# Kernel optimization log

Measured on AMD Instinct MI355X. Metric: run time of the kernel, lower is better.

## Reference

```python
import jax, jax.numpy as jnp
import numpy as np
from jax import lax

B, S, D, H = 8, 1024, 512, 8
K = 25  # moving-average kernel
EPS = 1e-6


def setup_inputs() -> dict:
    key = jax.random.key(0)
    ks = jax.random.split(key, 8)

    def dense_w(k, din, dout):
        return (jax.random.normal(k, (din, dout), jnp.float32) / np.sqrt(din).astype(np.float32))

    return {
        "x": jax.random.normal(ks[0], (B, S, D), jnp.float32),
        "wq": dense_w(ks[1], D, D), "bq": jnp.zeros((D,), jnp.float32),
        "wk": dense_w(ks[2], D, D), "bk": jnp.zeros((D,), jnp.float32),
        "wv": dense_w(ks[3], D, D), "bv": jnp.zeros((D,), jnp.float32),
        "wo": dense_w(ks[4], D, D), "bo": jnp.zeros((D,), jnp.float32),
        "w1": dense_w(ks[5], D, 4 * D), "b1": jnp.zeros((4 * D,), jnp.float32),
        "w2": dense_w(ks[6], 4 * D, D), "b2": jnp.zeros((D,), jnp.float32),
        "g1": jnp.ones((D,), jnp.float32), "be1": jnp.zeros((D,), jnp.float32),
        "g2": jnp.ones((D,), jnp.float32), "be2": jnp.zeros((D,), jnp.float32),
        "g3": jnp.ones((D,), jnp.float32), "be3": jnp.zeros((D,), jnp.float32),
        "num_heads": H,
    }


def _moving_avg(x):
    # TF AveragePooling1D(pool=K, stride=1, padding='same'): divisor excludes padding.
    s = lax.reduce_window(x, 0.0, lax.add, (1, K, 1), (1, 1, 1), 'SAME')
    cnt = lax.reduce_window(jnp.ones((1, x.shape[1], 1), x.dtype), 0.0, lax.add,
                            (1, K, 1), (1, 1, 1), 'SAME')
    return s / cnt


def _layernorm(x, g, b):
    m = jnp.mean(x, -1, keepdims=True)
    v = jnp.var(x, -1, keepdims=True)
    return (x - m) * jax.lax.rsqrt(v + EPS) * g + b


def _auto_correlation(x, wq, bq, wk, bk, wv, bv, wo, bo, num_heads):
    b, s, d = x.shape
    dp = d // num_heads
    def split_heads(t):
        return t.reshape(b, s, num_heads, dp).transpose(0, 2, 1, 3)  # [B,H,S,dp]
    q = split_heads(x @ wq + bq)
    k = split_heads(x @ wk + bk)
    v = split_heads(x @ wv + bv)
    # Faithful to source: rfft over innermost (depth) axis, fft_length = 2*S.
    qf = jnp.fft.rfft(q, n=2 * s, axis=-1)
    kf = jnp.fft.rfft(k, n=2 * s, axis=-1)
    corr = jnp.fft.irfft(qf * jnp.conj(kf), n=2 * s, axis=-1)[..., :s]  # [B,H,S,S]
    scale = 1.0 / np.sqrt(dp).astype(np.float32)
    attn = jax.nn.softmax(scale * corr, axis=-1)
    out = jnp.einsum('bhst,bhtd->bhsd', attn, v)
    out = out.transpose(0, 2, 1, 3).reshape(b, s, d)
    return out @ wo + bo


def reference(x, wq, bq, wk, bk, wv, bv, wo, bo, w1, b1, w2, b2,
              g1, be1, g2, be2, g3, be3, num_heads):
    trend_init = _moving_avg(x)
    seasonal_init = x - trend_init
    attn_out = _auto_correlation(seasonal_init, wq, bq, wk, bk, wv, bv, wo, bo, num_heads)
    out1 = _layernorm(attn_out + seasonal_init, g1, be1)
    ffn = jax.nn.relu(out1 @ w1 + b1) @ w2 + b2
    seasonal_out = _layernorm(out1 + ffn, g2, be2) + seasonal_init
    trend2 = _moving_avg(seasonal_out)
    seasonal_final = seasonal_out - trend2
    x_out = seasonal_final + (trend2 + trend_init)
    return _layernorm(x_out, g3, be3)
```

## Files before the change

### kernel.cpp

```cpp
#include <hip/hip_runtime.h>
#include <cstdint>


typedef float f32x4 __attribute__((ext_vector_type(4)));
typedef __bf16 bf16x8 __attribute__((ext_vector_type(8)));
typedef _Float16 h2t __attribute__((ext_vector_type(2)));
typedef unsigned short u16;
typedef unsigned int u32;
typedef u32 u32x4 __attribute__((ext_vector_type(4)));

__device__ __forceinline__ u16 f2bf(float f) {
  unsigned int u = __float_as_uint(f);
  u = (u + 0x7FFFu + ((u >> 16) & 1u)) >> 16;
  return (u16)u;
}

__device__ __forceinline__ float bf2f(u16 b) { return __uint_as_float((u32)b << 16); }

__device__ __forceinline__ u16 f2h(float f) {
  _Float16 hv = (_Float16)f;
  u16 b;
  __builtin_memcpy(&b, &hv, 2);
  return b;
}

__device__ __forceinline__ float dot2h(u32 qp, u32 kp_, float c) {
#if __has_builtin(__builtin_amdgcn_fdot2)
  return __builtin_amdgcn_fdot2(__builtin_bit_cast(h2t, qp),
                                __builtin_bit_cast(h2t, kp_), c, false);
#else
  h2t q = __builtin_bit_cast(h2t, qp), k = __builtin_bit_cast(h2t, kp_);
  c = fmaf((float)q.x, (float)k.x, c);
  return fmaf((float)q.y, (float)k.y, c);
#endif
}

__device__ __forceinline__ void gload_lds16(const void* g, void* l) {
  __builtin_amdgcn_global_load_lds((__attribute__((address_space(1))) void*)g,
                                   (__attribute__((address_space(3))) void*)l,
                                   16, 0, 0);
}

__global__ __launch_bounds__(256) void prep_kernel(
    const float* __restrict__ wq, const float* __restrict__ wk,
    const float* __restrict__ wv, const float* __restrict__ wo,
    const float* __restrict__ w1, const float* __restrict__ w2,
    const float* __restrict__ bq, const float* __restrict__ bk,
    u16* __restrict__ wqkt, u16* __restrict__ wvt, u16* __restrict__ wot,
    u16* __restrict__ w1t, u16* __restrict__ w2t, float* __restrict__ qkbias,
    const float* __restrict__ x, u16* __restrict__ seas_bf,
    u16* __restrict__ a64, float* __restrict__ srow) {
  __shared__ float tile[32][33];
  int i = blockIdx.x;
  int tid = threadIdx.x;
  int tx = tid & 31, ty = tid >> 5;
  if (i >= 3076) {
    int blk = i - 3076;
    int sc = blk & 127, b = blk >> 7;
    int d = tid * 2;
    const float* xb = x + (size_t)b * 1024 * 512 + d;
    int s0 = sc * 8;
    int lo = max(s0 - 12, 0), hi = min(s0 + 12, 1023);
    float sx = 0.f, sy = 0.f;
    for (int j = lo; j <= hi; ++j) {
      float2 v = *(const float2*)&xb[(size_t)j * 512];
      sx += v.x;
      sy += v.y;
    }
    float ax = 0.f, ay = 0.f;
#pragma unroll
    for (int s = s0; s < s0 + 8; ++s) {
      int l2 = max(s - 12, 0), h2 = min(s + 12, 1023);
      float invc = 1.f / (float)(h2 - l2 + 1);
      float2 xv = *(const float2*)&xb[(size_t)s * 512];
      float sex = xv.x - sx * invc;
      float sey = xv.y - sy * invc;
      size_t idx = (size_t)(b * 1024 + s) * 512 + d;
      u32 pk = (u32)f2bf(sex) | ((u32)f2bf(sey) << 16);
      *(u32*)&seas_bf[idx] = pk;
      if (s < 64) *(u32*)&a64[(size_t)(b * 64 + s) * 512 + d] = pk;
      ax += sex;
      ay += sey;
      if (s - 12 >= 0) {
        float2 v = *(const float2*)&xb[(size_t)(s - 12) * 512];
        sx -= v.x;
        sy -= v.y;
      }
      if (s + 13 <= 1023) {
        float2 v = *(const float2*)&xb[(size_t)(s + 13) * 512];
        sx += v.x;
        sy += v.y;
      }
    }
    atomicAdd(&srow[b * 512 + d], ax);
    atomicAdd(&srow[b * 512 + d + 1], ay);
    return;
  }
  if (i >= 3072) {
    int idx = (i - 3072) * 256 + tid;
    qkbias[idx] = idx < 512 ? bq[idx] : bk[idx - 512];
    return;
  }
  const float* src;
  u16* dst;
  int R, C, bx, by;
  if (i < 1024) {
    int w = i >> 8, l = i & 255;
    src = (w == 0 ? wq : w == 1 ? wk : w == 2 ? wv : wo);
    dst = (w == 0 ? wqkt : w == 1 ? wqkt + 512 * 512 : w == 2 ? wvt : wot);
    R = 512; C = 512; bx = l & 15; by = l >> 4;
  } else if (i < 2048) {
    int l = i - 1024;
    src = w1; dst = w1t; R = 512; C = 2048; bx = l & 15; by = l >> 4;
  } else {
    int l = i - 2048;
    src = w2; dst = w2t; R = 2048; C = 512; bx = l & 63; by = l >> 6;
  }
  int r0 = bx * 32, c0 = by * 32;
#pragma unroll
  for (int k = 0; k < 4; ++k)
    tile[ty + 8 * k][tx] = src[(size_t)(r0 + ty + 8 * k) * C + c0 + tx];
  __syncthreads();
#pragma unroll
  for (int k = 0; k < 4; ++k)
    dst[(size_t)(c0 + ty + 8 * k) * R + r0 + tx] = f2bf(tile[tx][ty + 8 * k]);
}

__global__ __launch_bounds__(256) void vsum_kernel(
    const float* __restrict__ srow, const float* __restrict__ wv,
    const float* __restrict__ bv, float* __restrict__ vsum) {
  int blk = blockIdx.x;
  int b = blk >> 1;
  int n = (blk & 1) * 256 + threadIdx.x;
  float a0 = 0.f, a1 = 0.f, a2 = 0.f, a3 = 0.f;
  float a4 = 0.f, a5 = 0.f, a6 = 0.f, a7 = 0.f;
  const float* sr = srow + b * 512;
  for (int k = 0; k < 512; k += 8) {
    a0 = fmaf(sr[k + 0], wv[(size_t)(k + 0) * 512 + n], a0);
    a1 = fmaf(sr[k + 1], wv[(size_t)(k + 1) * 512 + n], a1);
    a2 = fmaf(sr[k + 2], wv[(size_t)(k + 2) * 512 + n], a2);
    a3 = fmaf(sr[k + 3], wv[(size_t)(k + 3) * 512 + n], a3);
    a4 = fmaf(sr[k + 4], wv[(size_t)(k + 4) * 512 + n], a4);
    a5 = fmaf(sr[k + 5], wv[(size_t)(k + 5) * 512 + n], a5);
    a6 = fmaf(sr[k + 6], wv[(size_t)(k + 6) * 512 + n], a6);
    a7 = fmaf(sr[k + 7], wv[(size_t)(k + 7) * 512 + n], a7);
  }
  vsum[b * 512 + n] = ((a0 + a1) + (a2 + a3)) + ((a4 + a5) + (a6 + a7)) + 1024.f * bv[n];
}

template <int RELU, int OMODE, int KSPLIT>
__global__ __launch_bounds__(512, 1) void gemm8p_kernel(
    const u16* __restrict__ A, const u16* __restrict__ Bt,
    const float* __restrict__ bias, void* __restrict__ Cv, void* __restrict__ Cv2,
    int M, int N, int K) {
  __shared__ u16 As[3][2][256 * 32];
  __shared__ u16 Bs[3][2][128 * 32];
  const int tid = threadIdx.x;
  const int wid = tid >> 6, lane = tid & 63;
  const int wm = wid >> 2, wn = wid & 3;
  const int la = lane & 15, lg = lane >> 4;
  int nwg = gridDim.x * gridDim.y;
  int lin = blockIdx.y * gridDim.x + blockIdx.x;
  int swz = (lin & 7) * (nwg >> 3) + (lin >> 3);
  int bx = swz / gridDim.y, by = swz % gridDim.y;
  const int row0 = bx * 256, col0 = by * 128;
  const int z = (KSPLIT > 1) ? (int)blockIdx.z : 0;
  const int kbeg = z * (K / KSPLIT);
  const int nt = (K / KSPLIT) / 64;
  f32x4 acc[8][2] = {};

  auto stageh = [&](int buf, int h, int k0) {
    int kh = k0 + h * 32;
    {
      int p = tid, r = p >> 2, cg = (p & 3) ^ ((r >> 1) & 3);
      gload_lds16(A + (size_t)(row0 + r) * K + kh + cg * 8,
                  ((char*)&As[buf][h][0]) + p * 16);
    }
    {
      int p = tid + 512, r = p >> 2, cg = (p & 3) ^ ((r >> 1) & 3);
      gload_lds16(A + (size_t)(row0 + r) * K + kh + cg * 8,
                  ((char*)&As[buf][h][0]) + p * 16);
    }
    {
      int p = tid, r = p >> 2, cg = (p & 3) ^ ((r >> 1) & 3);
      gload_lds16(Bt + (size_t)(col0 + r) * K + kh + cg * 8,
                  ((char*)&Bs[buf][h][0]) + p * 16);
    }
  };

  stageh(0, 0, kbeg);
  stageh(0, 1, kbeg);
  stageh(1, 0, kbeg + 64);
  stageh(1, 1, kbeg + 64);
  asm volatile("s_waitcnt vmcnt(6)" ::: "memory");
  __builtin_amdgcn_s_barrier();
  __builtin_amdgcn_sched_barrier(0);

  for (int t = 0; t < nt; ++t) {
    const int buf = t % 3;
    const int nbuf = (t + 2) % 3;
    const bool pre = (t + 2 < nt);
#pragma unroll
    for (int h = 0; h < 2; ++h) {
      bf16x8 af[8], bf[2];
#pragma unroll
      for (int mf = 0; mf < 8; ++mf) {
        int r = wm * 128 + mf * 16 + la;
        int cp = lg ^ ((r >> 1) & 3);
        af[mf] = *(const bf16x8*)&As[buf][h][r * 32 + cp * 8];
      }
#pragma unroll
      for (int nf = 0; nf < 2; ++nf) {
        int r = wn * 32 + nf * 16 + la;
        int cp = lg ^ ((r >> 1) & 3);
        bf[nf] = *(const bf16x8*)&Bs[buf][h][r * 32 + cp * 8];
      }
      if (pre) stageh(nbuf, h, kbeg + (t + 2) * 64);
      __builtin_amdgcn_sched_barrier(0);
      __builtin_amdgcn_s_barrier();
      __builtin_amdgcn_s_setprio(1);
#pragma unroll
      for (int mf = 0; mf < 8; ++mf)
#pragma unroll
        for (int nf = 0; nf < 2; ++nf)
          acc[mf][nf] = __builtin_amdgcn_mfma_f32_16x16x32_bf16(af[mf], bf[nf], acc[mf][nf], 0, 0, 0);
      __builtin_amdgcn_s_setprio(0);
      __builtin_amdgcn_sched_barrier(0);
      if (h == 0) __builtin_amdgcn_s_barrier();
    }
    if (pre)
      asm volatile("s_waitcnt vmcnt(6)" ::: "memory");
    else if (t + 1 < nt)
      asm volatile("s_waitcnt vmcnt(0)" ::: "memory");
    __builtin_amdgcn_s_barrier();
    __builtin_amdgcn_sched_barrier(0);
  }

  void* Cout = (z == 0) ? Cv : Cv2;
#pragma unroll
  for (int mf = 0; mf < 8; ++mf) {
    int r = row0 + wm * 128 + mf * 16 + lg * 4;
#pragma unroll
    for (int nf = 0; nf < 2; ++nf) {
      int cc = col0 + wn * 32 + nf * 16 + la;
      float bvv = (z == 0) ? bias[cc] : 0.f;
#pragma unroll
      for (int j = 0; j < 4; ++j) {
        float v = acc[mf][nf][j] + bvv;
        if (RELU) v = fmaxf(v, 0.f);
        if constexpr (OMODE == 1)
          ((u16*)Cout)[(size_t)(r + j) * N + cc] = f2bf(v);
        else
          ((u16*)Cout)[(size_t)(r + j) * N + cc] = f2h(v);
      }
    }
  }
}

template <int RELU, int KSPLIT>
__global__ __launch_bounds__(512, 1) void gemmfp_kernel(
    const u16* __restrict__ A, const u16* __restrict__ Bt,
    const float* __restrict__ bias, u16* __restrict__ C0, u16* __restrict__ C1,
    u16* __restrict__ C2, u16* __restrict__ C3, int M, int N, int K) {
  __shared__ u16 As[2][2][256 * 32];
  __shared__ u16 Bs[2][2][256 * 32];
  const int tid = threadIdx.x;
  const int wid = tid >> 6, lane = tid & 63;
  const int wm = wid >> 2, wn = wid & 3;
  const int la = lane & 15, lg = lane >> 4;
  int nwg = gridDim.x * gridDim.y;
  int lin = blockIdx.y * gridDim.x + blockIdx.x;
  int swz = (lin & 7) * (nwg >> 3) + (lin >> 3);
  int bx = swz / gridDim.y, by = swz % gridDim.y;
  const int row0 = bx * 256, col0 = by * 256;
  const int z = (KSPLIT > 1) ? (int)blockIdx.z : 0;
  const int kbeg = z * (K / KSPLIT);
  const int nt = (K / KSPLIT) / 64;
  f32x4 acc[8][4] = {};

  auto stageA = [&](int d, int s, int k0) {
#pragma unroll
    for (int j = 0; j < 2; ++j) {
      int p = tid + j * 512;
      int r = p >> 2, cg = (p & 3) ^ ((r >> 1) & 3);
      gload_lds16(A + (size_t)(row0 + r) * K + k0 + s * 32 + cg * 8,
                  ((char*)&As[d][s][0]) + p * 16);
    }
  };
  auto stageB = [&](int d, int s, int k0) {
#pragma unroll
    for (int j = 0; j < 2; ++j) {
      int p = tid + j * 512;
      int r = p >> 2, cg = (p & 3) ^ ((r >> 1) & 3);
      gload_lds16(Bt + (size_t)(col0 + r) * K + k0 + s * 32 + cg * 8,
                  ((char*)&Bs[d][s][0]) + p * 16);
    }
  };

  stageA(0, 0, kbeg);
  stageB(0, 0, kbeg);
  stageA(0, 1, kbeg);
  stageB(0, 1, kbeg);
  asm volatile("s_waitcnt vmcnt(0)" ::: "memory");
  __builtin_amdgcn_s_barrier();
  __builtin_amdgcn_sched_barrier(0);

  for (int t = 0; t < nt; ++t) {
    const int d = t & 1, nd = d ^ 1;
    const int k1 = kbeg + (t + 1) * 64;
    const bool pre = (t + 1 < nt);
    bf16x8 af[8], bf[2];
#pragma unroll
    for (int s = 0; s < 2; ++s) {
#pragma unroll
      for (int mf = 0; mf < 8; ++mf) {
        int r = wm * 128 + mf * 16 + la;
        int cp = lg ^ ((r >> 1) & 3);
        af[mf] = *(const bf16x8*)(((const char*)&As[d][s][0]) + r * 64 + cp * 16);
      }
#pragma unroll
      for (int nf = 0; nf < 2; ++nf) {
        int r = wn * 64 + nf * 16 + la;
        int cp = lg ^ ((r >> 1) & 3);
        bf[nf] = *(const bf16x8*)(((const char*)&Bs[d][s][0]) + r * 64 + cp * 16);
      }
      if (pre) stageA(nd, s, k1);
      __builtin_amdgcn_sched_barrier(0);
      __builtin_amdgcn_s_barrier();
      asm volatile("s_waitcnt lgkmcnt(0)" ::: "memory");
      __builtin_amdgcn_sched_barrier(0);
      __builtin_amdgcn_s_setprio(1);
#pragma unroll
      for (int mf = 0; mf < 8; ++mf)
#pragma unroll
        for (int nf = 0; nf < 2; ++nf)
          acc[mf][nf] = __builtin_amdgcn_mfma_f32_16x16x32_bf16(af[mf], bf[nf], acc[mf][nf], 0, 0, 0);
      __builtin_amdgcn_s_setprio(0);
      __builtin_amdgcn_sched_barrier(0);
      __builtin_amdgcn_s_barrier();
#pragma unroll
      for (int nf = 0; nf < 2; ++nf) {
        int r = wn * 64 + (nf + 2) * 16 + la;
        int cp = lg ^ ((r >> 1) & 3);
        bf[nf] = *(const bf16x8*)(((const char*)&Bs[d][s][0]) + r * 64 + cp * 16);
      }
      if (pre) stageB(nd, s, k1);
      __builtin_amdgcn_sched_barrier(0);
      if (pre)
        asm volatile("s_waitcnt vmcnt(4)" ::: "memory");
      else
        asm volatile("s_waitcnt vmcnt(0)" ::: "memory");
      __builtin_amdgcn_s_barrier();
      asm volatile("s_waitcnt lgkmcnt(0)" ::: "memory");
      __builtin_amdgcn_sched_barrier(0);
      __builtin_amdgcn_s_setprio(1);
#pragma unroll
      for (int mf = 0; mf < 8; ++mf)
#pragma unroll
        for (int nf = 0; nf < 2; ++nf)
          acc[mf][nf + 2] = __builtin_amdgcn_mfma_f32_16x16x32_bf16(af[mf], bf[nf], acc[mf][nf + 2], 0, 0, 0);
      __builtin_amdgcn_s_setprio(0);
      __builtin_amdgcn_sched_barrier(0);
      __builtin_amdgcn_s_barrier();
    }
  }

  u16* Cout = (z == 0) ? C0 : (z == 1) ? C1 : (z == 2) ? C2 : C3;
#pragma unroll
  for (int mf = 0; mf < 8; ++mf) {
    int r = row0 + wm * 128 + mf * 16 + lg * 4;
#pragma unroll
    for (int nf = 0; nf < 4; ++nf) {
      int cc = col0 + wn * 64 + nf * 16 + la;
      float bvv = (z == 0) ? bias[cc] : 0.f;
#pragma unroll
      for (int j = 0; j < 4; ++j) {
        float v = acc[mf][nf][j] + bvv;
        if (RELU) v = fmaxf(v, 0.f);
        Cout[(size_t)(r + j) * N + cc] = f2bf(v);
      }
    }
  }
}

__global__ __launch_bounds__(256, 6) void gemm_v_kernel(
    const u16* __restrict__ A, const u16* __restrict__ Bt,
    const float* __restrict__ bias, u16* __restrict__ Cv, int M, int N, int K) {
  constexpr int BK = 32;
  __shared__ u16 As[2][128 * BK];
  __shared__ u16 Bs[2][64 * BK];
  const int tid = threadIdx.x;
  const int wid = tid >> 6, lane = tid & 63;
  const int wm = wid >> 1, wn = wid & 1;
  const int la = lane & 15, lg = lane >> 4;
  const int row0 = blockIdx.x * 128, col0 = blockIdx.y * 64;
  const int ksteps = K / BK;
  f32x4 acc[4][2] = {};

  auto stage = [&](int buf, int k0) {
    {
      int p = tid, r = p >> 2, cg = (p & 3) ^ ((r >> 1) & 3);
      gload_lds16(A + (size_t)(row0 + r) * K + k0 + cg * 8, ((char*)As[buf]) + p * 16);
    }
    {
      int p = tid + 256, r = p >> 2, cg = (p & 3) ^ ((r >> 1) & 3);
      gload_lds16(A + (size_t)(row0 + r) * K + k0 + cg * 8, ((char*)As[buf]) + p * 16);
    }
    {
      int p = tid, r = p >> 2, cg = (p & 3) ^ ((r >> 1) & 3);
      gload_lds16(Bt + (size_t)(col0 + r) * K + k0 + cg * 8, ((char*)Bs[buf]) + p * 16);
    }
  };

  stage(0, 0);
  __syncthreads();
  for (int t = 0; t < ksteps; ++t) {
    const int cur = t & 1;
    if (t + 1 < ksteps) stage(cur ^ 1, (t + 1) * BK);
    bf16x8 af[4], bfr[2];
#pragma unroll
    for (int m = 0; m < 4; ++m) {
      int r = wm * 64 + m * 16 + la;
      int cp = lg ^ ((r >> 1) & 3);
      af[m] = *(const bf16x8*)(((const char*)As[cur]) + r * 64 + cp * 16);
    }
#pragma unroll
    for (int n = 0; n < 2; ++n) {
      int r = wn * 32 + n * 16 + la;
      int cp = lg ^ ((r >> 1) & 3);
      bfr[n] = *(const bf16x8*)(((const char*)Bs[cur]) + r * 64 + cp * 16);
    }
#pragma unroll
    for (int m = 0; m < 4; ++m)
#pragma unroll
      for (int n = 0; n < 2; ++n)
        acc[m][n] = __builtin_amdgcn_mfma_f32_16x16x32_bf16(af[m], bfr[n], acc[m][n], 0, 0, 0);
    __syncthreads();
  }

#pragma unroll
  for (int m = 0; m < 4; ++m) {
    int r = row0 + wm * 64 + m * 16 + lg * 4;
#pragma unroll
    for (int n = 0; n < 2; ++n) {
      int cc = col0 + wn * 32 + n * 16 + la;
      float bvv = bias[cc];
#pragma unroll
      for (int j = 0; j < 4; ++j) {
        float v = acc[m][n][j] + bvv;
        int rr = r + j;
        int bb = rr >> 6, tt = rr & 63, hh = cc >> 6, dd = cc & 63;
        Cv[(((size_t)bb * 8 + hh) * 64 + dd) * 64 + tt] = f2bf(v);
      }
    }
  }
}

__global__ __launch_bounds__(256) void attn_mfma_kernel(
    const u16* __restrict__ qk, const u16* __restrict__ v64t,
    const float* __restrict__ vsum, u16* __restrict__ attn_bf) {
  __shared__ u32 qE[16][64];
  __shared__ u32 qO[16][64];
  __shared__ u32 kp[16][32];
  __shared__ u16 coef[16][64];
  __shared__ u16 vtt[64][64];
  __shared__ float zc[16];
  __shared__ float Vs[64];
  int bid = blockIdx.x;
  int scnk = bid & 63, h = (bid >> 6) & 7, b = bid >> 9;
  int tid = threadIdx.x, wid = tid >> 6, lane = tid & 63;
  int bh = b * 8 + h;
  int row0 = b * 1024 + scnk * 16;

  {
    int p = tid, r = p >> 3, cc = p & 7;
    gload_lds16(v64t + ((size_t)bh * 4096 + r * 64 + ((cc ^ (r & 7)) * 8)),
                ((char*)vtt) + p * 16);
    p = tid + 256; r = p >> 3; cc = p & 7;
    gload_lds16(v64t + ((size_t)bh * 4096 + r * 64 + ((cc ^ (r & 7)) * 8)),
                ((char*)vtt) + p * 16);
  }
  for (int idx = tid; idx < 512; idx += 256) {
    int s = idx >> 5, j = (idx & 31) + 32;
    qE[s][j] = 0;
  }
  {
    if (tid < 128) {
      int s = tid >> 3, c = tid & 7;
      size_t grow = ((size_t)(row0 + s)) * 1024 + h * 64;
      *(f32x4*)&qE[s][c * 4] = *(const f32x4*)&qk[grow + c * 8];
    } else {
      int t2 = tid - 128;
      int s = t2 >> 3, c = t2 & 7;
      size_t grow = ((size_t)(row0 + s)) * 1024 + 512 + h * 64;
      *(f32x4*)&kp[s][c * 4] = *(const f32x4*)&qk[grow + c * 8];
    }
  }
  if (tid < 64) Vs[tid] = vsum[b * 512 + h * 64 + tid];
  __syncthreads();
  for (int idx = tid; idx < 512; idx += 256) {
    int s = idx >> 5, j = idx & 31;
    u32 a = qE[s][j], b2 = qE[s][j + 1];
    qO[s][j] = (a >> 16) | (b2 << 16);
    qO[s][j + 32] = 0;
  }
  __syncthreads();
  for (int i = 0; i < 4; ++i) {
    int s = wid * 4 + i;
    u32x4 kk4[8];
#pragma unroll
    for (int u = 0; u < 8; ++u) kk4[u] = *(const u32x4*)&kp[s][u * 4];
    int t = lane, sel = t & 1;
    const u32* qptr = (sel ? qO[s] : qE[s]) + (t >> 1);
    float c = 0.f;
#pragma unroll
    for (int u = 0; u < 8; ++u) {
#pragma unroll
      for (int v = 0; v < 4; ++v) c = dot2h(qptr[u * 4 + v], kk4[u][v], c);
    }
    float sc = c * 0.125f;
    float mx = fmaxf(sc, 0.f);
#pragma unroll
    for (int off = 32; off >= 1; off >>= 1) mx = fmaxf(mx, __shfl_xor(mx, off));
    float w = __expf(sc - mx), wz = __expf(-mx);
    float sw = w;
#pragma unroll
    for (int off = 32; off >= 1; off >>= 1) sw += __shfl_xor(sw, off);
    float inv = 1.f / (sw + 960.f * wz);
    *(u16*)(((char*)&coef[s][0]) + ((2 * t) ^ ((s & 7) << 4))) = f2bf((w - wz) * inv);
    if (lane == 0) zc[s] = wz * inv;
  }
  __syncthreads();
  {
    int la = lane & 15, lg = lane >> 4;
    int r = la;
    int n0 = wid * 16 + la;
    f32x4 a0 = {};
#pragma unroll
    for (int ks = 0; ks < 2; ++ks) {
      int lr = ks * 4 + lg;
      bf16x8 af = *(const bf16x8*)(((const char*)coef) + r * 128 + ((lr ^ (r & 7)) << 4));
      bf16x8 b0 = *(const bf16x8*)(((const char*)vtt) + n0 * 128 + ((lr ^ (n0 & 7)) << 4));
      a0 = __builtin_amdgcn_mfma_f32_16x16x32_bf16(af, b0, a0, 0, 0, 0);
    }
    int srl0 = lg * 4;
    float vs0 = Vs[wid * 16 + la];
#pragma unroll
    for (int j = 0; j < 4; ++j) {
      size_t rb = (size_t)(row0 + srl0 + j) * 512 + h * 64;
      attn_bf[rb + wid * 16 + la] = f2bf(a0[j] + zc[srl0 + j] * vs0);
    }
  }
}

__device__ __forceinline__ void block_reduce_2(float& a, float& b, float* sbuf) {
  int tid = threadIdx.x, wid = tid >> 6, lane = tid & 63;
#pragma unroll
  for (int off = 32; off >= 1; off >>= 1) {
    a += __shfl_xor(a, off);
    b += __shfl_xor(b, off);
  }
  if (lane == 0) {
    sbuf[wid] = a;
    sbuf[4 + wid] = b;
  }
  __syncthreads();
  a = sbuf[0] + sbuf[1] + sbuf[2] + sbuf[3];
  b = sbuf[4] + sbuf[5] + sbuf[6] + sbuf[7];
  __syncthreads();
}

__global__ __launch_bounds__(256) void ln_res_kernel(
    const u16* __restrict__ xa, const u16* __restrict__ xb,
    u16* __restrict__ res_out,
    const float* __restrict__ g, const float* __restrict__ be) {
  __shared__ float sbuf[8];
  int row = blockIdx.x, tid = threadIdx.x;
  int d = tid * 2;
  size_t base = (size_t)row * 512 + d;
  u32 pa = *(const u32*)&xa[base];
  u32 pb = *(const u32*)&xb[base];
  u32 pr = *(const u32*)&res_out[base];
  float v0 = bf2f((u16)pa) + bf2f((u16)pb) + bf2f((u16)pr);
  float v1 = bf2f((u16)(pa >> 16)) + bf2f((u16)(pb >> 16)) + bf2f((u16)(pr >> 16));
  float s = v0 + v1, q = v0 * v0 + v1 * v1;
  block_reduce_2(s, q, sbuf);
  float mean = s * (1.f / 512.f);
  float var = q * (1.f / 512.f) - mean * mean;
  float rs = rsqrtf(var + 1e-6f);
  float2 gg = *(const float2*)&g[d];
  float2 bb = *(const float2*)&be[d];
  float o0 = (v0 - mean) * rs * gg.x + bb.x;
  float o1 = (v1 - mean) * rs * gg.y + bb.y;
  *(u32*)&res_out[base] = (u32)f2bf(o0) | ((u32)f2bf(o1) << 16);
}

__global__ __launch_bounds__(256) void final_kernel(
    const u16* __restrict__ out1, const u16* __restrict__ fa,
    const u16* __restrict__ fb, const u16* __restrict__ fc,
    const u16* __restrict__ fd, const float* __restrict__ x,
    const float* __restrict__ g2, const float* __restrict__ be2,
    const float* __restrict__ g3, const float* __restrict__ be3,
    float* __restrict__ out) {
  __shared__ float sbuf[8];
  int row = blockIdx.x, tid = threadIdx.x;
  int d = tid * 2;
  size_t base = (size_t)row * 512 + d;
  u32 po = *(const u32*)&out1[base];
  u32 pa = *(const u32*)&fa[base];
  u32 pb = *(const u32*)&fb[base];
  u32 pc = *(const u32*)&fc[base];
  u32 pd = *(const u32*)&fd[base];
  float t0 = bf2f((u16)po) + bf2f((u16)pa) + bf2f((u16)pb) + bf2f((u16)pc) + bf2f((u16)pd);
  float t1 = bf2f((u16)(po >> 16)) + bf2f((u16)(pa >> 16)) + bf2f((u16)(pb >> 16)) +
             bf2f((u16)(pc >> 16)) + bf2f((u16)(pd >> 16));
  float s = t0 + t1, q = t0 * t0 + t1 * t1;
  block_reduce_2(s, q, sbuf);
  float mean = s * (1.f / 512.f);
  float var = q * (1.f / 512.f) - mean * mean;
  float rs = rsqrtf(var + 1e-6f);
  float2 g2v = *(const float2*)&g2[d];
  float2 b2v = *(const float2*)&be2[d];
  float2 xv = *(const float2*)&x[base];
  float y0 = (t0 - mean) * rs * g2v.x + b2v.x + xv.x;
  float y1 = (t1 - mean) * rs * g2v.y + b2v.y + xv.y;
  s = y0 + y1;
  q = y0 * y0 + y1 * y1;
  block_reduce_2(s, q, sbuf);
  mean = s * (1.f / 512.f);
  var = q * (1.f / 512.f) - mean * mean;
  rs = rsqrtf(var + 1e-6f);
  float2 g3v = *(const float2*)&g3[d];
  float2 b3v = *(const float2*)&be3[d];
  float2 o = make_float2((y0 - mean) * rs * g3v.x + b3v.x,
                         (y1 - mean) * rs * g3v.y + b3v.y);
  *(float2*)&out[base] = o;
}

extern "C" void kernel_launch(void* const* d_in, const int* in_sizes, int n_in,
                              void* d_out, int out_size, void* d_ws, size_t ws_size,
                              hipStream_t stream) {
  const float* x = (const float*)d_in[0];
  const float* wq = (const float*)d_in[1];
  const float* bq = (const float*)d_in[2];
  const float* wk = (const float*)d_in[3];
  const float* bk = (const float*)d_in[4];
  const float* wv = (const float*)d_in[5];
  const float* bv = (const float*)d_in[6];
  const float* wo = (const float*)d_in[7];
  const float* bo = (const float*)d_in[8];
  const float* w1 = (const float*)d_in[9];
  const float* b1 = (const float*)d_in[10];
  const float* w2 = (const float*)d_in[11];
  const float* b2 = (const float*)d_in[12];
  const float* g1 = (const float*)d_in[13];
  const float* be1 = (const float*)d_in[14];
  const float* g2 = (const float*)d_in[15];
  const float* be2 = (const float*)d_in[16];
  const float* g3 = (const float*)d_in[17];
  const float* be3 = (const float*)d_in[18];
  float* out = (float*)d_out;

  const size_t MS = 8192ull * 512ull;
  float* srow = (float*)d_ws;
  float* vsumb = srow + 4096;
  float* qkbias = vsumb + 4096;
  u16* qk_f16 = (u16*)(qkbias + 1024);
  u16* hidden = qk_f16 + 8192ull * 1024;
  u16* seas_bf = hidden + 8192ull * 2048;
  u16* attn_bf = seas_bf + MS;
  u16* wo0 = attn_bf + MS;
  u16* wo1 = wo0 + MS;
  u16* v64t = wo1 + MS;
  u16* a64_bf = v64t + 512 * 512;
  u16* wqkt = a64_bf + 512 * 512;
  u16* wvt = wqkt + 1024 * 512;
  u16* wot = wvt + 512 * 512;
  u16* w1t = wot + 512 * 512;
  u16* w2t = w1t + 2048ull * 512;
  u16* ff0 = qk_f16;
  u16* ff1 = ff0 + MS;
  u16* ff2 = wo0;
  u16* ff3 = wo1;

  hipMemsetAsync(srow, 0, 4096 * sizeof(float), stream);
  prep_kernel<<<4100, 256, 0, stream>>>(
      wq, wk, wv, wo, w1, w2, bq, bk, wqkt, wvt, wot, w1t, w2t, qkbias,
      x, seas_bf, a64_bf, srow);
  vsum_kernel<<<16, 256, 0, stream>>>(srow, wv, bv, vsumb);

  gemm8p_kernel<0, 2, 1><<<dim3(32, 8), 512, 0, stream>>>(
      seas_bf, wqkt, qkbias, qk_f16, nullptr, 8192, 1024, 512);
  gemm_v_kernel<<<dim3(4, 8), 256, 0, stream>>>(a64_bf, wvt, bv, v64t, 512, 512, 512);

  attn_mfma_kernel<<<4096, 256, 0, stream>>>(qk_f16, v64t, vsumb, attn_bf);

  gemm8p_kernel<0, 1, 2><<<dim3(32, 4, 2), 512, 0, stream>>>(
      attn_bf, wot, bo, wo0, wo1, 8192, 512, 512);
  ln_res_kernel<<<8192, 256, 0, stream>>>(wo0, wo1, seas_bf, g1, be1);

  gemmfp_kernel<1, 1><<<dim3(32, 8), 512, 0, stream>>>(
      seas_bf, w1t, b1, hidden, nullptr, nullptr, nullptr, 8192, 2048, 512);
  gemmfp_kernel<0, 4><<<dim3(32, 2, 4), 512, 0, stream>>>(
      hidden, w2t, b2, ff0, ff1, ff2, ff3, 8192, 512, 2048);

  final_kernel<<<8192, 256, 0, stream>>>(seas_bf, ff0, ff1, ff2, ff3, x,
                                         g2, be2, g3, be3, out);
}
```

Baseline: 199.1 us.

## Fuse QK GEMM, V GEMM and vsum into one kernel; drop atomics

```diff
diff --git a/kernel.cpp b/kernel.cpp
--- a/kernel.cpp
+++ b/kernel.cpp
@@ -49,7 +49,7 @@
     u16* __restrict__ wqkt, u16* __restrict__ wvt, u16* __restrict__ wot,
     u16* __restrict__ w1t, u16* __restrict__ w2t, float* __restrict__ qkbias,
     const float* __restrict__ x, u16* __restrict__ seas_bf,
-    u16* __restrict__ a64, float* __restrict__ srow) {
+    u16* __restrict__ a64, float* __restrict__ srow_part) {
   __shared__ float tile[32][33];
   int i = blockIdx.x;
   int tid = threadIdx.x;
@@ -92,8 +92,7 @@
         sy += v.y;
       }
     }
-    atomicAdd(&srow[b * 512 + d], ax);
-    atomicAdd(&srow[b * 512 + d + 1], ay);
+    *(float2*)&srow_part[(size_t)sc * 4096 + b * 512 + d] = make_float2(ax, ay);
     return;
   }
   if (i >= 3072) {
@@ -126,26 +125,183 @@
     dst[(size_t)(c0 + ty + 8 * k) * R + r0 + tx] = f2bf(tile[tx][ty + 8 * k]);
 }
 
-__global__ __launch_bounds__(256) void vsum_kernel(
-    const float* __restrict__ srow, const float* __restrict__ wv,
-    const float* __restrict__ bv, float* __restrict__ vsum) {
-  int blk = blockIdx.x;
-  int b = blk >> 1;
-  int n = (blk & 1) * 256 + threadIdx.x;
-  float a0 = 0.f, a1 = 0.f, a2 = 0.f, a3 = 0.f;
-  float a4 = 0.f, a5 = 0.f, a6 = 0.f, a7 = 0.f;
-  const float* sr = srow + b * 512;
-  for (int k = 0; k < 512; k += 8) {
-    a0 = fmaf(sr[k + 0], wv[(size_t)(k + 0) * 512 + n], a0);
-    a1 = fmaf(sr[k + 1], wv[(size_t)(k + 1) * 512 + n], a1);
-    a2 = fmaf(sr[k + 2], wv[(size_t)(k + 2) * 512 + n], a2);
-    a3 = fmaf(sr[k + 3], wv[(size_t)(k + 3) * 512 + n], a3);
-    a4 = fmaf(sr[k + 4], wv[(size_t)(k + 4) * 512 + n], a4);
-    a5 = fmaf(sr[k + 5], wv[(size_t)(k + 5) * 512 + n], a5);
-    a6 = fmaf(sr[k + 6], wv[(size_t)(k + 6) * 512 + n], a6);
-    a7 = fmaf(sr[k + 7], wv[(size_t)(k + 7) * 512 + n], a7);
-  }
-  vsum[b * 512 + n] = ((a0 + a1) + (a2 + a3)) + ((a4 + a5) + (a6 + a7)) + 1024.f * bv[n];
+__global__ __launch_bounds__(512, 1) void qkv_kernel(
+    const u16* __restrict__ A, const u16* __restrict__ Wqk,
+    const float* __restrict__ qkbias, u16* __restrict__ qk_f16,
+    const u16* __restrict__ a64, const u16* __restrict__ Wvt,
+    const float* __restrict__ bv, u16* __restrict__ v64t,
+    const float* __restrict__ srow_part, const float* __restrict__ wv,
+    float* __restrict__ vsum) {
+  __shared__ u16 As[3][2][256 * 32];
+  __shared__ u16 Bs[3][2][128 * 32];
+  const int bid = blockIdx.x;
+  const int tid = threadIdx.x;
+  const int wid = tid >> 6, lane = tid & 63;
+  const int la = lane & 15, lg = lane >> 4;
+
+  if (bid >= 288) {
+    float* ssrow = (float*)As;
+    int b = bid - 288, n = tid;
+    float acc = 0.f;
+    for (int c = 0; c < 128; ++c) acc += srow_part[(size_t)c * 4096 + b * 512 + n];
+    ssrow[n] = acc;
+    __syncthreads();
+    float a0 = 0.f, a1 = 0.f, a2 = 0.f, a3 = 0.f;
+    for (int k = 0; k < 512; k += 4) {
+      a0 = fmaf(ssrow[k + 0], wv[(size_t)(k + 0) * 512 + n], a0);
+      a1 = fmaf(ssrow[k + 1], wv[(size_t)(k + 1) * 512 + n], a1);
+      a2 = fmaf(ssrow[k + 2], wv[(size_t)(k + 2) * 512 + n], a2);
+      a3 = fmaf(ssrow[k + 3], wv[(size_t)(k + 3) * 512 + n], a3);
+    }
+    vsum[b * 512 + n] = (a0 + a1) + (a2 + a3) + 1024.f * bv[n];
+    return;
+  }
+
+  if (bid >= 256) {
+    u16* As2 = (u16*)As;
+    u16* Bs2 = As2 + 2 * 128 * 32;
+    int vb = bid - 256;
+    const int row0 = (vb & 3) * 128, col0 = (vb >> 2) * 64;
+    const int wm = wid >> 2, wn = wid & 3;
+    f32x4 acc[4] = {};
+    auto stage = [&](int buf, int k0) {
+      {
+        int p = tid, r = p >> 2, cg = (p & 3) ^ ((r >> 1) & 3);
+        gload_lds16(a64 + (size_t)(row0 + r) * 512 + k0 + cg * 8,
+                    ((char*)(As2 + buf * 128 * 32)) + p * 16);
+      }
+      if (tid < 256) {
+        int p = tid, r = p >> 2, cg = (p & 3) ^ ((r >> 1) & 3);
+        gload_lds16(Wvt + (size_t)(col0 + r) * 512 + k0 + cg * 8,
+                    ((char*)(Bs2 + buf * 64 * 32)) + p * 16);
+      }
+    };
+    stage(0, 0);
+    __syncthreads();
+    for (int t = 0; t < 16; ++t) {
+      const int cur = t & 1;
+      if (t + 1 < 16) stage(cur ^ 1, (t + 1) * 32);
+      bf16x8 af[4], bfv;
+#pragma unroll
+      for (int m = 0; m < 4; ++m) {
+        int r = wm * 64 + m * 16 + la;
+        int cp = lg ^ ((r >> 1) & 3);
+        af[m] = *(const bf16x8*)(((const char*)(As2 + cur * 128 * 32)) + r * 64 + cp * 16);
+      }
+      {
+        int r = wn * 16 + la;
+        int cp = lg ^ ((r >> 1) & 3);
+        bfv = *(const bf16x8*)(((const char*)(Bs2 + cur * 64 * 32)) + r * 64 + cp * 16);
+      }
+#pragma unroll
+      for (int m = 0; m < 4; ++m)
+        acc[m] = __builtin_amdgcn_mfma_f32_16x16x32_bf16(af[m], bfv, acc[m], 0, 0, 0);
+      __syncthreads();
+    }
+#pragma unroll
+    for (int m = 0; m < 4; ++m) {
+      int r = row0 + wm * 64 + m * 16 + lg * 4;
+      int cc = col0 + wn * 16 + la;
+      float bvv = bv[cc];
+#pragma unroll
+      for (int j = 0; j < 4; ++j) {
+        float v = acc[m][j] + bvv;
+        int rr = r + j;
+        int bb = rr >> 6, tt = rr & 63, hh = cc >> 6, dd = cc & 63;
+        v64t[(((size_t)bb * 8 + hh) * 64 + dd) * 64 + tt] = f2bf(v);
+      }
+    }
+    return;
+  }
+
+  const int K = 512, N = 1024;
+  const int wm = wid >> 2, wn = wid & 3;
+  int lin = bid;
+  int swz = (lin & 7) * 32 + (lin >> 3);
+  int bx = swz >> 3, by = swz & 7;
+  const int row0 = bx * 256, col0 = by * 128;
+  const int nt = 8;
+  f32x4 acc[8][2] = {};
+
+  auto stageh = [&](int buf, int h, int k0) {
+    int kh = k0 + h * 32;
+    {
+      int p = tid, r = p >> 2, cg = (p & 3) ^ ((r >> 1) & 3);
+      gload_lds16(A + (size_t)(row0 + r) * K + kh + cg * 8,
+                  ((char*)&As[buf][h][0]) + p * 16);
+    }
+    {
+      int p = tid + 512, r = p >> 2, cg = (p & 3) ^ ((r >> 1) & 3);
+      gload_lds16(A + (size_t)(row0 + r) * K + kh + cg * 8,
+                  ((char*)&As[buf][h][0]) + p * 16);
+    }
+    {
+      int p = tid, r = p >> 2, cg = (p & 3) ^ ((r >> 1) & 3);
+      gload_lds16(Wqk + (size_t)(col0 + r) * K + kh + cg * 8,
+                  ((char*)&Bs[buf][h][0]) + p * 16);
+    }
+  };
+
+  stageh(0, 0, 0);
+  stageh(0, 1, 0);
+  stageh(1, 0, 64);
+  stageh(1, 1, 64);
+  asm volatile("s_waitcnt vmcnt(6)" ::: "memory");
+  __builtin_amdgcn_s_barrier();
+  __builtin_amdgcn_sched_barrier(0);
+
+  for (int t = 0; t < nt; ++t) {
+    const int buf = t % 3;
+    const int nbuf = (t + 2) % 3;
+    const bool pre = (t + 2 < nt);
+#pragma unroll
+    for (int h = 0; h < 2; ++h) {
+      bf16x8 af[8], bf[2];
+#pragma unroll
+      for (int mf = 0; mf < 8; ++mf) {
+        int r = wm * 128 + mf * 16 + la;
+        int cp = lg ^ ((r >> 1) & 3);
+        af[mf] = *(const bf16x8*)&As[buf][h][r * 32 + cp * 8];
+      }
+#pragma unroll
+      for (int nf = 0; nf < 2; ++nf) {
+        int r = wn * 32 + nf * 16 + la;
+        int cp = lg ^ ((r >> 1) & 3);
+        bf[nf] = *(const bf16x8*)&Bs[buf][h][r * 32 + cp * 8];
+      }
+      if (pre) stageh(nbuf, h, (t + 2) * 64);
+      __builtin_amdgcn_sched_barrier(0);
+      __builtin_amdgcn_s_barrier();
+      __builtin_amdgcn_s_setprio(1);
+#pragma unroll
+      for (int mf = 0; mf < 8; ++mf)
+#pragma unroll
+        for (int nf = 0; nf < 2; ++nf)
+          acc[mf][nf] = __builtin_amdgcn_mfma_f32_16x16x32_bf16(af[mf], bf[nf], acc[mf][nf], 0, 0, 0);
+      __builtin_amdgcn_s_setprio(0);
+      __builtin_amdgcn_sched_barrier(0);
+      if (h == 0) __builtin_amdgcn_s_barrier();
+    }
+    if (pre)
+      asm volatile("s_waitcnt vmcnt(6)" ::: "memory");
+    else if (t + 1 < nt)
+      asm volatile("s_waitcnt vmcnt(0)" ::: "memory");
+    __builtin_amdgcn_s_barrier();
+    __builtin_amdgcn_sched_barrier(0);
+  }
+
+#pragma unroll
+  for (int mf = 0; mf < 8; ++mf) {
+    int r = row0 + wm * 128 + mf * 16 + lg * 4;
+#pragma unroll
+    for (int nf = 0; nf < 2; ++nf) {
+      int cc = col0 + wn * 32 + nf * 16 + la;
+      float bvv = qkbias[cc];
+#pragma unroll
+      for (int j = 0; j < 4; ++j)
+        qk_f16[(size_t)(r + j) * N + cc] = f2h(acc[mf][nf][j] + bvv);
+    }
+  }
 }
 
 template <int RELU, int OMODE, int KSPLIT>
@@ -378,79 +534,6 @@
         float v = acc[mf][nf][j] + bvv;
         if (RELU) v = fmaxf(v, 0.f);
         Cout[(size_t)(r + j) * N + cc] = f2bf(v);
-      }
-    }
-  }
-}
-
-__global__ __launch_bounds__(256, 6) void gemm_v_kernel(
-    const u16* __restrict__ A, const u16* __restrict__ Bt,
-    const float* __restrict__ bias, u16* __restrict__ Cv, int M, int N, int K) {
-  constexpr int BK = 32;
-  __shared__ u16 As[2][128 * BK];
-  __shared__ u16 Bs[2][64 * BK];
-  const int tid = threadIdx.x;
-  const int wid = tid >> 6, lane = tid & 63;
-  const int wm = wid >> 1, wn = wid & 1;
-  const int la = lane & 15, lg = lane >> 4;
-  const int row0 = blockIdx.x * 128, col0 = blockIdx.y * 64;
-  const int ksteps = K / BK;
-  f32x4 acc[4][2] = {};
-
-  auto stage = [&](int buf, int k0) {
-    {
-      int p = tid, r = p >> 2, cg = (p & 3) ^ ((r >> 1) & 3);
-      gload_lds16(A + (size_t)(row0 + r) * K + k0 + cg * 8, ((char*)As[buf]) + p * 16);
-    }
-    {
-      int p = tid + 256, r = p >> 2, cg = (p & 3) ^ ((r >> 1) & 3);
-      gload_lds16(A + (size_t)(row0 + r) * K + k0 + cg * 8, ((char*)As[buf]) + p * 16);
-    }
-    {
-      int p = tid, r = p >> 2, cg = (p & 3) ^ ((r >> 1) & 3);
-      gload_lds16(Bt + (size_t)(col0 + r) * K + k0 + cg * 8, ((char*)Bs[buf]) + p * 16);
-    }
-  };
-
-  stage(0, 0);
-  __syncthreads();
-  for (int t = 0; t < ksteps; ++t) {
-    const int cur = t & 1;
-    if (t + 1 < ksteps) stage(cur ^ 1, (t + 1) * BK);
-    bf16x8 af[4], bfr[2];
-#pragma unroll
-    for (int m = 0; m < 4; ++m) {
-      int r = wm * 64 + m * 16 + la;
-      int cp = lg ^ ((r >> 1) & 3);
-      af[m] = *(const bf16x8*)(((const char*)As[cur]) + r * 64 + cp * 16);
-    }
-#pragma unroll
-    for (int n = 0; n < 2; ++n) {
-      int r = wn * 32 + n * 16 + la;
-      int cp = lg ^ ((r >> 1) & 3);
-      bfr[n] = *(const bf16x8*)(((const char*)Bs[cur]) + r * 64 + cp * 16);
-    }
-#pragma unroll
-    for (int m = 0; m < 4; ++m)
-#pragma unroll
-      for (int n = 0; n < 2; ++n)
-        acc[m][n] = __builtin_amdgcn_mfma_f32_16x16x32_bf16(af[m], bfr[n], acc[m][n], 0, 0, 0);
-    __syncthreads();
-  }
-
-#pragma unroll
-  for (int m = 0; m < 4; ++m) {
-    int r = row0 + wm * 64 + m * 16 + lg * 4;
-#pragma unroll
-    for (int n = 0; n < 2; ++n) {
-      int cc = col0 + wn * 32 + n * 16 + la;
-      float bvv = bias[cc];
-#pragma unroll
-      for (int j = 0; j < 4; ++j) {
-        float v = acc[m][n][j] + bvv;
-        int rr = r + j;
-        int bb = rr >> 6, tt = rr & 63, hh = cc >> 6, dd = cc & 63;
-        Cv[(((size_t)bb * 8 + hh) * 64 + dd) * 64 + tt] = f2bf(v);
       }
     }
   }
@@ -662,8 +745,8 @@
   float* out = (float*)d_out;
 
   const size_t MS = 8192ull * 512ull;
-  float* srow = (float*)d_ws;
-  float* vsumb = srow + 4096;
+  float* srow_part = (float*)d_ws;
+  float* vsumb = srow_part + 524288;
   float* qkbias = vsumb + 4096;
   u16* qk_f16 = (u16*)(qkbias + 1024);
   u16* hidden = qk_f16 + 8192ull * 1024;
@@ -683,15 +766,13 @@
   u16* ff2 = wo0;
   u16* ff3 = wo1;
 
-  hipMemsetAsync(srow, 0, 4096 * sizeof(float), stream);
   prep_kernel<<<4100, 256, 0, stream>>>(
       wq, wk, wv, wo, w1, w2, bq, bk, wqkt, wvt, wot, w1t, w2t, qkbias,
-      x, seas_bf, a64_bf, srow);
-  vsum_kernel<<<16, 256, 0, stream>>>(srow, wv, bv, vsumb);
-
-  gemm8p_kernel<0, 2, 1><<<dim3(32, 8), 512, 0, stream>>>(
-      seas_bf, wqkt, qkbias, qk_f16, nullptr, 8192, 1024, 512);
-  gemm_v_kernel<<<dim3(4, 8), 256, 0, stream>>>(a64_bf, wvt, bv, v64t, 512, 512, 512);
+      x, seas_bf, a64_bf, srow_part);
+
+  qkv_kernel<<<296, 512, 0, stream>>>(
+      seas_bf, wqkt, qkbias, qk_f16, a64_bf, wvt, bv, v64t,
+      srow_part, wv, vsumb);
 
   attn_mfma_kernel<<<4096, 256, 0, stream>>>(qk_f16, v64t, vsumb, attn_bf);
 
```

New measurement: 182.3 us. 1.09x faster.
